# Optimization experiments

Hardware: AMD Instinct MI355X
Metric: run time of the kernel (lower is better)

Reference implementation:

```python
import jax, jax.numpy as jnp
import numpy as np

B, L = 8, 512
D_MODEL, N_HEAD, N_GLOBAL, N_ITER = 64, 8, 64, 4
DAMP_H = 0.0; DAMP_Z = 0.0; STEP_H = 1.0; STEP_Z = 1.0; REG_H = 1.0; REG_Z = 1.0
NEG = -1e9; BIG = 1e9


def sin_pe(length, d):
    # standard additive sinusoidal positional encoding (AddPositionalEncoding)
    pos = np.arange(length, dtype=np.float32)[:, None]
    div = np.exp(np.arange(0, d, 2, dtype=np.float32) * (-np.log(10000.0) / d))
    pe = np.zeros((length, d), dtype=np.float32)
    pe[:, 0::2] = np.sin(pos * div)
    pe[:, 1::2] = np.cos(pos * div)
    return jnp.asarray(pe)


def setup_inputs() -> dict:
    key = jax.random.key(0)
    k1, k2, k3 = jax.random.split(key, 3)
    x = jax.random.normal(k1, (B, L, D_MODEL), jnp.float32)
    mask = jnp.ones((B, L), jnp.int32)
    ternary = jax.random.normal(k2, (D_MODEL, D_MODEL, N_HEAD), jnp.float32)  # std=1 init
    global_w = jax.random.normal(k3, (N_GLOBAL, D_MODEL, 1), jnp.float32) / np.sqrt(D_MODEL)
    return {"x": x, "mask": mask, "ternary": ternary, "global_w": global_w}


def _forward(x, mask, ternary, global_w):
    Bq, Lq, d = x.shape
    norm = lambda a: jax.nn.softmax(a, axis=-1)
    valid = (mask != 0)
    m1 = valid[:, :, None].astype(x.dtype)                      # (B,L,1) keep-mask
    pair = valid[:, None, :, None] & valid[:, None, None, :]    # (B,1,L,L)
    eye_big = BIG * jnp.eye(Lq, dtype=x.dtype)[None, None]      # kill self-edges

    x = x + sin_pe(Lq, d)[None]
    unary = x * m1
    q_z = unary
    q_h1 = jnp.where(pair, 1.0 - eye_big, NEG)                  # (B,H,L,L) via broadcast
    q_h1 = jnp.broadcast_to(q_h1, (Bq, N_HEAD, Lq, Lq))
    q_h2 = jnp.ones((Bq, 1, Lq, N_GLOBAL), x.dtype)             # single-channel: 1 global head

    cache_qh1, cache_qh2 = q_h1, q_h2
    cache_norm_qz = norm(q_z)
    cache_norm_qh1 = norm(q_h1)
    cache_norm_qh2 = norm(q_h2)

    for it in range(N_ITER):
        cache_qz = q_z
        nz = norm(q_z)
        qzn = nz if it == 0 else (1 - STEP_Z) * cache_norm_qz + STEP_Z * nz
        cache_norm_qz = qzn
        qz = qzn * m1
        # F1[z,c,i,j] = sum_{a,b} qz[z,i,a] qz[z,j,b] T[a,b,c]
        t1 = jnp.einsum('zia,abc->zibc', qz, ternary)
        F1 = jnp.einsum('zibc,zjb->zcij', t1, qz)
        F2 = jnp.einsum('zia,jac->zcij', qz, global_w)          # (B,1,L,n_global)
        q_h1 = cache_qh1 * DAMP_H + F1 * (1 - DAMP_H)
        q_h2 = cache_qh2 * DAMP_H + F2 * (1 - DAMP_H)
        cache_qh1, cache_qh2 = q_h1, q_h2
        q_h1m = jnp.where(pair, q_h1 - eye_big, NEG)
        nh1 = norm(q_h1m / REG_H)
        nh2 = norm(q_h2 / REG_H)
        qh1n = nh1 if it == 0 else (1 - STEP_H) * cache_norm_qh1 + STEP_H * nh1
        qh2n = nh2 if it == 0 else (1 - STEP_H) * cache_norm_qh2 + STEP_H * nh2
        cache_norm_qh1, cache_norm_qh2 = qh1n, qh2n
        # messages back to Z: factor (H_i=c, Z_i=a, Z_j=b)
        mi = jnp.einsum('zcij,zjb->zicb', qh1n, qz)
        Mi = jnp.einsum('zicb,abc->zia', mi, ternary)           # to Z_i
        mj = jnp.einsum('zcij,zia->zjca', qh1n, qz)
        Mj = jnp.einsum('zjca,abc->zjb', mj, ternary)           # to Z_j (block_msg=False)
        Mg = jnp.einsum('zcij,jac->zia', qh2n, global_w)        # global-node message
        new_qz = (unary + (Mi + Mj + Mg) / REG_Z) * m1
        q_z = cache_qz * DAMP_Z + new_qz * (1 - DAMP_Z)
    return q_z  # output_prob=False -> unnormalized scores (B,L,d_model)


def reference(x, mask, ternary, global_w):
    return _forward(x, mask, ternary, global_w)
```

## Files before the change

### kernel.cpp

```cpp
#include <hip/hip_runtime.h>

#define BB 8
#define LL 512
#define HH 8
#define BIGV (1e9f)

typedef unsigned short u16;
typedef __attribute__((ext_vector_type(8))) short bf16x8;
typedef __attribute__((ext_vector_type(4))) short s16x4;
typedef __attribute__((ext_vector_type(4))) float f32x4;

#define MFMA(a,b,c) __builtin_amdgcn_mfma_f32_16x16x32_bf16(a,b,c,0,0,0)

__device__ __forceinline__ u16 f2b(float f){
  unsigned u = __float_as_uint(f);
  u = (u + 0x7fffu + ((u>>16)&1u)) >> 16;
  return (u16)u;
}
__device__ __forceinline__ float b2f(u16 s){ return __uint_as_float(((unsigned)s)<<16); }
__device__ __forceinline__ bf16x8 ldb8(const u16* p){ return *(const bf16x8*)p; }
__device__ __forceinline__ s16x4 ld4nt(const u16* p){ return __builtin_nontemporal_load((const s16x4*)p); }

__device__ __forceinline__ float g16_sum(float v){
  v += __shfl_xor(v,1,64); v += __shfl_xor(v,2,64);
  v += __shfl_xor(v,4,64); v += __shfl_xor(v,8,64);
  return v;
}

__global__ void kp_prep(const float* __restrict__ T, const float* __restrict__ gw,
                        u16* __restrict__ T4t, u16* __restrict__ Tt2,
                        u16* __restrict__ Gt, u16* __restrict__ Gt2){
  int idx = blockIdx.x*256 + threadIdx.x;
  { int c=idx>>12, b=(idx>>6)&63, a=idx&63; T4t[idx] = f2b(T[(a*64+b)*8+c]); }
  { int c=idx>>12, a=(idx>>6)&63, b=idx&63; Tt2[idx] = f2b(T[(a*64+b)*8+c]); }
  if(idx < 4096){
    int a=idx>>6, j=idx&63;
    Gt[idx]  = f2b(gw[j*64+a]);
    Gt2[idx] = f2b(gw[idx]);
  }
}

__global__ __launch_bounds__(256) void kCA(const float* __restrict__ x, const int* __restrict__ mask,
      const u16* __restrict__ miP, const u16* __restrict__ mjP, const float* __restrict__ MgF_in,
      float* __restrict__ unary, float* __restrict__ mf,
      const u16* __restrict__ Gt2, const u16* __restrict__ Gt,
      u16* __restrict__ qzb, float* __restrict__ MgF_out, float* __restrict__ out, int mode){
  __shared__ u16 qlds[16*72];
  __shared__ u16 P2s[16*72];
  __shared__ float red2[16*4];
  int bid = blockIdx.x; int z = bid & 7, itile = bid >> 3;
  int t = threadIdx.x, lane = t&63, w = t>>6, l15 = lane&15, lhi = lane>>4;
  int rbase = z*LL + itile*16;
  {
    int row16 = t>>4, c4 = t&15;
    int rg = rbase + row16;
    float v[4]; float mk;
    if(mode == 0){
      mk = (mask[rg] != 0) ? 1.f : 0.f;
      if(c4 == 0) mf[rg] = mk;
      int pos = rg & (LL-1);
      #pragma unroll
      for(int k=0;k<4;k++){
        int d = c4*4 + k;
        float div = __expf(-(float)(d & ~1) * 0.14391156962f);
        float arg = (float)pos * div;
        float pe = (d & 1) ? cosf(arg) : sinf(arg);
        v[k] = (x[(size_t)rg*64 + d] + pe) * mk;
      }
      *(f32x4*)&unary[(size_t)rg*64 + c4*4] = (f32x4){v[0],v[1],v[2],v[3]};
    } else {
      mk = mf[rg];
      f32x4 acc = *(const f32x4*)&MgF_in[(size_t)rg*64 + c4*4];
      #pragma unroll
      for(int c=0;c<8;c++){
        s16x4 vv = ld4nt(&miP[(size_t)rg*512 + c*64 + c4*4]);
        acc[0]+=b2f((u16)vv[0]); acc[1]+=b2f((u16)vv[1]);
        acc[2]+=b2f((u16)vv[2]); acc[3]+=b2f((u16)vv[3]);
      }
      #pragma unroll
      for(int s=0;s<4;s++)
        #pragma unroll
        for(int c=0;c<8;c++){
          s16x4 vv = ld4nt(&mjP[(((size_t)(s*8+z))*LL + itile*16 + row16)*512 + c*64 + c4*4]);
          acc[0]+=b2f((u16)vv[0]); acc[1]+=b2f((u16)vv[1]);
          acc[2]+=b2f((u16)vv[2]); acc[3]+=b2f((u16)vv[3]);
        }
      f32x4 u0 = *(const f32x4*)&unary[(size_t)rg*64 + c4*4];
      #pragma unroll
      for(int k=0;k<4;k++) v[k] = (u0[k] + acc[k]) * mk;
    }
    if(mode == 2){
      *(f32x4*)&out[(size_t)rg*64 + c4*4] = (f32x4){v[0],v[1],v[2],v[3]};
      return;
    }
    float mx = fmaxf(fmaxf(v[0],v[1]), fmaxf(v[2],v[3]));
    mx = fmaxf(mx, __shfl_xor(mx,1,64));
    mx = fmaxf(mx, __shfl_xor(mx,2,64));
    mx = fmaxf(mx, __shfl_xor(mx,4,64));
    mx = fmaxf(mx, __shfl_xor(mx,8,64));
    float s = 0.f;
    #pragma unroll
    for(int k=0;k<4;k++){ v[k] = __expf(v[k]-mx); s += v[k]; }
    s += __shfl_xor(s,1,64); s += __shfl_xor(s,2,64);
    s += __shfl_xor(s,4,64); s += __shfl_xor(s,8,64);
    float iv = mk / s;
    s16x4 q4 = { (short)f2b(v[0]*iv), (short)f2b(v[1]*iv),
                 (short)f2b(v[2]*iv), (short)f2b(v[3]*iv) };
    *(s16x4*)&qzb[(size_t)rg*64 + c4*4] = q4;
    *(s16x4*)&qlds[row16*72 + c4*4] = q4;
  }
  __syncthreads();
  float fv[4];
  {
    bf16x8 a0 = ldb8(&qlds[l15*72 + lhi*8]);
    bf16x8 a1 = ldb8(&qlds[l15*72 + lhi*8 + 32]);
    const u16* Br = Gt2 + (size_t)(w*16 + l15)*64 + lhi*8;
    f32x4 acc = {0.f,0.f,0.f,0.f};
    acc = MFMA(a0, ldb8(Br), acc);
    acc = MFMA(a1, ldb8(Br+32), acc);
    #pragma unroll
    for(int jj=0;jj<4;jj++){
      float e = __expf(acc[jj]);
      fv[jj] = e;
      float p = g16_sum(e);
      if(l15==0) red2[(lhi*4+jj)*4 + w] = p;
    }
  }
  __syncthreads();
  #pragma unroll
  for(int jj=0;jj<4;jj++){
    int r = lhi*4+jj;
    float s = red2[r*4+0]+red2[r*4+1]+red2[r*4+2]+red2[r*4+3];
    float iv = 1.f/s;
    P2s[r*72 + w*16 + l15] = f2b(fv[jj]*iv);
  }
  __syncthreads();
  {
    bf16x8 a0 = ldb8(&P2s[l15*72 + lhi*8]);
    bf16x8 a1 = ldb8(&P2s[l15*72 + lhi*8 + 32]);
    const u16* Br = Gt + (size_t)(w*16 + l15)*64 + lhi*8;
    f32x4 acc = {0.f,0.f,0.f,0.f};
    acc = MFMA(a0, ldb8(Br), acc);
    acc = MFMA(a1, ldb8(Br+32), acc);
    #pragma unroll
    for(int jj=0;jj<4;jj++)
      MgF_out[((size_t)rbase + lhi*4 + jj)*64 + w*16 + l15] = acc[jj];
  }
}

__global__ __launch_bounds__(256) void k2(const u16* __restrict__ qzb,
      const u16* __restrict__ T4t, const u16* __restrict__ Tt2,
      u16* __restrict__ t1b, u16* __restrict__ t1t, u16* __restrict__ t2t){
  __shared__ u16 s1[64*72];
  __shared__ u16 s2[64*72];
  __shared__ u16 s3[64*72];
  int bid = blockIdx.x; int z = bid&7, c = (bid>>3)&7, itile = bid>>6;
  int zc = z*8 + c;
  int t = threadIdx.x, lane = t&63, w = t>>6, l15 = lane&15, lhi = lane>>4;
  int i0 = itile*64;
  const u16* qA = qzb + ((size_t)z*LL + i0 + w*16 + l15)*64 + lhi*8;
  bf16x8 qa0 = ldb8(qA), qa1 = ldb8(qA+32);
  const u16* tA = T4t + c*4096 + (w*16 + l15)*64 + lhi*8;
  bf16x8 ta0 = ldb8(tA), ta1 = ldb8(tA+32);
  const u16* uA = Tt2 + c*4096 + (w*16 + l15)*64 + lhi*8;
  bf16x8 ua0 = ldb8(uA), ua1 = ldb8(uA+32);
  #pragma unroll
  for(int nt=0;nt<4;nt++){
    {
      const u16* Br = T4t + c*4096 + (nt*16 + l15)*64 + lhi*8;
      f32x4 acc = {0.f,0.f,0.f,0.f};
      acc = MFMA(qa0, ldb8(Br), acc);
      acc = MFMA(qa1, ldb8(Br+32), acc);
      #pragma unroll
      for(int jj=0;jj<4;jj++)
        s1[(w*16 + lhi*4 + jj)*72 + nt*16 + l15] = f2b(acc[jj]);
    }
    const u16* Br = qzb + ((size_t)z*LL + i0 + nt*16 + l15)*64 + lhi*8;
    bf16x8 qb0 = ldb8(Br), qb1 = ldb8(Br+32);
    {
      f32x4 acc = {0.f,0.f,0.f,0.f};
      acc = MFMA(ta0, qb0, acc);
      acc = MFMA(ta1, qb1, acc);
      #pragma unroll
      for(int jj=0;jj<4;jj++)
        s2[(w*16 + lhi*4 + jj)*72 + nt*16 + l15] = f2b(acc[jj]);
    }
    {
      f32x4 acc = {0.f,0.f,0.f,0.f};
      acc = MFMA(ua0, qb0, acc);
      acc = MFMA(ua1, qb1, acc);
      #pragma unroll
      for(int jj=0;jj<4;jj++)
        s3[(w*16 + lhi*4 + jj)*72 + nt*16 + l15] = f2b(acc[jj]);
    }
  }
  __syncthreads();
  #pragma unroll
  for(int p=0;p<2;p++){
    int r = p*32 + (t>>3), ch = t&7;
    *(bf16x8*)&t1b[((size_t)zc*LL + i0 + r)*64 + ch*8]   = *(const bf16x8*)&s1[r*72 + ch*8];
    *(bf16x8*)&t1t[((size_t)zc*64 + r)*LL + i0 + ch*8]   = *(const bf16x8*)&s2[r*72 + ch*8];
    *(bf16x8*)&t2t[((size_t)zc*64 + r)*LL + i0 + ch*8]   = *(const bf16x8*)&s3[r*72 + ch*8];
  }
}

__global__ __launch_bounds__(1024) void kF(const u16* __restrict__ t1b, const u16* __restrict__ qzb,
        const u16* __restrict__ t1t, const u16* __restrict__ t2t, const float* __restrict__ mf,
        u16* __restrict__ miP, u16* __restrict__ mjP){
  extern __shared__ char smem[];
  u16*   t2s  = (u16*)smem;
  u16*   Pp   = (u16*)(smem + 66560);
  u16*   PpT  = (u16*)(smem + 99840);
  float* redS2= (float*)(smem + 140800);
  float* stgf = (float*)(smem + 141056);
  u16*   stg  = (u16*)smem;
  int bid = blockIdx.x;
  int z = bid&7, c = (bid>>3)&7, it = bid>>6;
  int zc = z*8 + c;
  int t = threadIdx.x, lane = t&63, w = t>>6, l15 = lane&15, lhi = lane>>4;
  int jc0 = w*32;
  int h = w>>3, wr = (w>>2)&1, wc = w&3;
  if(t < 64) redS2[t] = 0.f;
  __syncthreads();
  #pragma unroll
  for(int m=0;m<4;m++){
    int e = (m*1024 + t)*8;
    int a = e >> 9, j = e & 511;
    *(bf16x8*)&t2s[a*520 + j] = ldb8(t2t + ((size_t)zc*64 + a)*LL + j);
  }
  float mfj[2];
  mfj[0] = mf[z*LL + jc0 + l15];
  mfj[1] = mf[z*LL + jc0 + 16 + l15];
  f32x4 mj[2][4];
  #pragma unroll
  for(int jt=0;jt<2;jt++)
    #pragma unroll
    for(int bt=0;bt<4;bt++) mj[jt][bt] = (f32x4){0.f,0.f,0.f,0.f};
  u16* PpTw = PpT + w*32*40;

  for(int ip=0; ip<4; ++ip){
    int i0g = it*128 + ip*32;
    int par = ip & 1;
    f32x4 S[2][2];
    #pragma unroll
    for(int rt=0;rt<2;rt++){ S[rt][0] = (f32x4){0,0,0,0}; S[rt][1] = (f32x4){0,0,0,0}; }
    #pragma unroll
    for(int rt=0;rt<2;rt++){
      const u16* Ar = t1b + ((size_t)zc*LL + i0g + rt*16 + l15)*64 + lhi*8;
      bf16x8 a0 = ldb8(Ar), a1 = ldb8(Ar+32);
      #pragma unroll
      for(int ct=0;ct<2;ct++){
        const u16* Br = qzb + ((size_t)z*LL + jc0 + ct*16 + l15)*64 + lhi*8;
        S[rt][ct] = MFMA(a0, ldb8(Br), S[rt][ct]);
        S[rt][ct] = MFMA(a1, ldb8(Br+32), S[rt][ct]);
      }
    }
    #pragma unroll
    for(int rt=0;rt<2;rt++)
      #pragma unroll
      for(int jj=0;jj<4;jj++){
        int rloc = rt*16 + lhi*4 + jj;
        int irow = i0g + rloc;
        float mfi = mf[z*LL + irow];
        float ps = 0.f;
        #pragma unroll
        for(int ct=0;ct<2;ct++){
          int jcol = jc0 + ct*16 + l15;
          float v = S[rt][ct][jj] - ((irow==jcol)?BIGV:0.f);
          float e = mfi * mfj[ct] * __expf(v);
          S[rt][ct][jj] = e; ps += e;
          Pp[rloc*520 + jcol] = f2b(e);
        }
        ps = g16_sum(ps);
        if(l15 == 0) atomicAdd(&redS2[par*32 + rloc], ps);
      }
    __syncthreads();
    if(t < 32) redS2[(par^1)*32 + t] = 0.f;
    float ivv[2][4];
    #pragma unroll
    for(int rt=0;rt<2;rt++)
      #pragma unroll
      for(int jj=0;jj<4;jj++){
        float s = redS2[par*32 + rt*16 + lhi*4 + jj];
        ivv[rt][jj] = s > 0.f ? 1.f/s : 0.f;
      }
    #pragma unroll
    for(int rt=0;rt<2;rt++)
      #pragma unroll
      for(int ct=0;ct<2;ct++){
        s16x4 v4 = { (short)f2b(S[rt][ct][0]*ivv[rt][0]), (short)f2b(S[rt][ct][1]*ivv[rt][1]),
                     (short)f2b(S[rt][ct][2]*ivv[rt][2]), (short)f2b(S[rt][ct][3]*ivv[rt][3]) };
        *(s16x4*)&PpTw[(ct*16 + l15)*40 + rt*16 + lhi*4] = v4;
      }
    {
      f32x4 mia = {0.f,0.f,0.f,0.f};
      const u16* Ab = Pp + (wr*16 + l15)*520 + h*256 + lhi*8;
      const u16* Bb = t2s + (wc*16 + l15)*520 + h*256 + lhi*8;
      #pragma unroll
      for(int ks=0;ks<8;ks++)
        mia = MFMA(ldb8(Ab + ks*32), ldb8(Bb + ks*32), mia);
      #pragma unroll
      for(int jj=0;jj<4;jj++)
        stgf[(h*32 + wr*16 + lhi*4 + jj)*68 + wc*16 + l15] = mia[jj]*ivv[wr][jj];
    }
    {
      bf16x8 av[2];
      #pragma unroll
      for(int jt=0;jt<2;jt++)
        av[jt] = ldb8(PpTw + (jt*16 + l15)*40 + lhi*8);
      #pragma unroll
      for(int bt=0;bt<4;bt++){
        bf16x8 b = ldb8(t1t + ((size_t)zc*64 + bt*16 + l15)*LL + i0g + lhi*8);
        #pragma unroll
        for(int jt=0;jt<2;jt++) mj[jt][bt] = MFMA(av[jt], b, mj[jt][bt]);
      }
    }
    __syncthreads();
    if(t < 512){
      int r = t>>4, cc = t&15;
      f32x4 v0 = *(const f32x4*)&stgf[r*68 + cc*4];
      f32x4 v1 = *(const f32x4*)&stgf[(32+r)*68 + cc*4];
      s16x4 o = { (short)f2b(v0[0]+v1[0]), (short)f2b(v0[1]+v1[1]),
                  (short)f2b(v0[2]+v1[2]), (short)f2b(v0[3]+v1[3]) };
      *(s16x4*)&miP[((size_t)z*LL + i0g + r)*512 + c*64 + cc*4] = o;
    }
  }
  #pragma unroll
  for(int jt=0;jt<2;jt++)
    #pragma unroll
    for(int bt=0;bt<4;bt++)
      #pragma unroll
      for(int jj=0;jj<4;jj++)
        stg[(jc0 + jt*16 + lhi*4 + jj)*72 + bt*16 + l15] = f2b(mj[jt][bt][jj]);
  __syncthreads();
  #pragma unroll
  for(int q=0;q<4;q++){
    int e = q*1024 + t;
    int j = e >> 3, ch = e & 7;
    *(bf16x8*)&mjP[(((size_t)(it*8 + z))*LL + j)*512 + c*64 + ch*8]
      = *(const bf16x8*)&stg[j*72 + ch*8];
  }
}

extern "C" void kernel_launch(void* const* d_in, const int* in_sizes, int n_in,
                              void* d_out, int out_size, void* d_ws, size_t ws_size,
                              hipStream_t stream) {
  const float* x       = (const float*)d_in[0];
  const int*   mask    = (const int*)d_in[1];
  const float* ternary = (const float*)d_in[2];
  const float* gw      = (const float*)d_in[3];
  float* out = (float*)d_out;

  const size_t NE = (size_t)BB*LL*64;
  char* p = (char*)d_ws;
  auto alloc = [&](size_t bytes)->void*{
    void* r = (void*)p; p += (bytes + 255) & ~(size_t)255; return r;
  };
  float* unary   = (float*)alloc(NE*4);
  float* mf      = (float*)alloc((size_t)BB*LL*4);
  u16*   qzb     = (u16*)alloc(NE*2);
  u16*   t1b     = (u16*)alloc((size_t)BB*HH*LL*64*2);
  u16*   t1t     = (u16*)alloc((size_t)BB*HH*LL*64*2);
  u16*   t2t     = (u16*)alloc((size_t)BB*HH*LL*64*2);
  float* MgF     = (float*)alloc(NE*4);
  u16*   miP     = (u16*)alloc((size_t)BB*LL*512*2);
  u16*   mjP     = (u16*)alloc((size_t)32*LL*512*2);
  u16*   T4t     = (u16*)alloc(32768*2);
  u16*   Tt2     = (u16*)alloc(32768*2);
  u16*   Gt      = (u16*)alloc(4096*2);
  u16*   Gt2     = (u16*)alloc(4096*2);

  const int KF_LDS = 158464;
  hipFuncSetAttribute(reinterpret_cast<const void*>(kF),
                      hipFuncAttributeMaxDynamicSharedMemorySize, KF_LDS);

  kp_prep<<<128, 256, 0, stream>>>(ternary, gw, T4t, Tt2, Gt, Gt2);
  kCA<<<256, 256, 0, stream>>>(x, mask, miP, mjP, MgF, unary, mf, Gt2, Gt,
                               qzb, MgF, out, 0);
  for(int it=0; it<4; ++it){
    k2<<<512, 256, 0, stream>>>(qzb, T4t, Tt2, t1b, t1t, t2t);
    kF<<<256, 1024, KF_LDS, stream>>>(t1b, qzb, t1t, t2t, mf, miP, mjP);
    kCA<<<256, 256, 0, stream>>>(x, mask, miP, mjP, MgF, unary, mf, Gt2, Gt,
                                 qzb, MgF, out, (it==3) ? 2 : 1);
  }
}
```

Baseline: 218.8 us.

## Fuse t1/t2 projection kernel into softmax kernel kCA using 512 threads

```diff
diff --git a/kernel.cpp b/kernel.cpp
--- a/kernel.cpp
+++ b/kernel.cpp
@@ -40,18 +40,20 @@
   }
 }
 
-__global__ __launch_bounds__(256) void kCA(const float* __restrict__ x, const int* __restrict__ mask,
+__global__ __launch_bounds__(512) void kCA(const float* __restrict__ x, const int* __restrict__ mask,
       const u16* __restrict__ miP, const u16* __restrict__ mjP, const float* __restrict__ MgF_in,
       float* __restrict__ unary, float* __restrict__ mf,
       const u16* __restrict__ Gt2, const u16* __restrict__ Gt,
-      u16* __restrict__ qzb, float* __restrict__ MgF_out, float* __restrict__ out, int mode){
+      const u16* __restrict__ T4t, const u16* __restrict__ Tt2,
+      u16* __restrict__ qzb, float* __restrict__ MgF_out, float* __restrict__ out,
+      u16* __restrict__ t1b, u16* __restrict__ t1t, u16* __restrict__ t2t, int mode){
   __shared__ u16 qlds[16*72];
   __shared__ u16 P2s[16*72];
   __shared__ float red2[16*4];
   int bid = blockIdx.x; int z = bid & 7, itile = bid >> 3;
   int t = threadIdx.x, lane = t&63, w = t>>6, l15 = lane&15, lhi = lane>>4;
   int rbase = z*LL + itile*16;
-  {
+  if(t < 256){
     int row16 = t>>4, c4 = t&15;
     int rg = rbase + row16;
     float v[4]; float mk;
@@ -91,27 +93,28 @@
     }
     if(mode == 2){
       *(f32x4*)&out[(size_t)rg*64 + c4*4] = (f32x4){v[0],v[1],v[2],v[3]};
-      return;
-    }
-    float mx = fmaxf(fmaxf(v[0],v[1]), fmaxf(v[2],v[3]));
-    mx = fmaxf(mx, __shfl_xor(mx,1,64));
-    mx = fmaxf(mx, __shfl_xor(mx,2,64));
-    mx = fmaxf(mx, __shfl_xor(mx,4,64));
-    mx = fmaxf(mx, __shfl_xor(mx,8,64));
-    float s = 0.f;
-    #pragma unroll
-    for(int k=0;k<4;k++){ v[k] = __expf(v[k]-mx); s += v[k]; }
-    s += __shfl_xor(s,1,64); s += __shfl_xor(s,2,64);
-    s += __shfl_xor(s,4,64); s += __shfl_xor(s,8,64);
-    float iv = mk / s;
-    s16x4 q4 = { (short)f2b(v[0]*iv), (short)f2b(v[1]*iv),
-                 (short)f2b(v[2]*iv), (short)f2b(v[3]*iv) };
-    *(s16x4*)&qzb[(size_t)rg*64 + c4*4] = q4;
-    *(s16x4*)&qlds[row16*72 + c4*4] = q4;
-  }
+    } else {
+      float mx = fmaxf(fmaxf(v[0],v[1]), fmaxf(v[2],v[3]));
+      mx = fmaxf(mx, __shfl_xor(mx,1,64));
+      mx = fmaxf(mx, __shfl_xor(mx,2,64));
+      mx = fmaxf(mx, __shfl_xor(mx,4,64));
+      mx = fmaxf(mx, __shfl_xor(mx,8,64));
+      float s = 0.f;
+      #pragma unroll
+      for(int k=0;k<4;k++){ v[k] = __expf(v[k]-mx); s += v[k]; }
+      s += __shfl_xor(s,1,64); s += __shfl_xor(s,2,64);
+      s += __shfl_xor(s,4,64); s += __shfl_xor(s,8,64);
+      float iv = mk / s;
+      s16x4 q4 = { (short)f2b(v[0]*iv), (short)f2b(v[1]*iv),
+                   (short)f2b(v[2]*iv), (short)f2b(v[3]*iv) };
+      *(s16x4*)&qzb[(size_t)rg*64 + c4*4] = q4;
+      *(s16x4*)&qlds[row16*72 + c4*4] = q4;
+    }
+  }
+  if(mode == 2) return;
   __syncthreads();
   float fv[4];
-  {
+  if(t < 256){
     bf16x8 a0 = ldb8(&qlds[l15*72 + lhi*8]);
     bf16x8 a1 = ldb8(&qlds[l15*72 + lhi*8 + 32]);
     const u16* Br = Gt2 + (size_t)(w*16 + l15)*64 + lhi*8;
@@ -127,15 +130,17 @@
     }
   }
   __syncthreads();
-  #pragma unroll
-  for(int jj=0;jj<4;jj++){
-    int r = lhi*4+jj;
-    float s = red2[r*4+0]+red2[r*4+1]+red2[r*4+2]+red2[r*4+3];
-    float iv = 1.f/s;
-    P2s[r*72 + w*16 + l15] = f2b(fv[jj]*iv);
-  }
-  __syncthreads();
-  {
+  if(t < 256){
+    #pragma unroll
+    for(int jj=0;jj<4;jj++){
+      int r = lhi*4+jj;
+      float s = red2[r*4+0]+red2[r*4+1]+red2[r*4+2]+red2[r*4+3];
+      float iv = 1.f/s;
+      P2s[r*72 + w*16 + l15] = f2b(fv[jj]*iv);
+    }
+  }
+  __syncthreads();
+  if(t < 256){
     bf16x8 a0 = ldb8(&P2s[l15*72 + lhi*8]);
     bf16x8 a1 = ldb8(&P2s[l15*72 + lhi*8 + 32]);
     const u16* Br = Gt + (size_t)(w*16 + l15)*64 + lhi*8;
@@ -146,61 +151,36 @@
     for(int jj=0;jj<4;jj++)
       MgF_out[((size_t)rbase + lhi*4 + jj)*64 + w*16 + l15] = acc[jj];
   }
-}
-
-__global__ __launch_bounds__(256) void k2(const u16* __restrict__ qzb,
-      const u16* __restrict__ T4t, const u16* __restrict__ Tt2,
-      u16* __restrict__ t1b, u16* __restrict__ t1t, u16* __restrict__ t2t){
-  __shared__ u16 s1[64*72];
-  __shared__ u16 s2[64*72];
-  __shared__ u16 s3[64*72];
-  int bid = blockIdx.x; int z = bid&7, c = (bid>>3)&7, itile = bid>>6;
-  int zc = z*8 + c;
-  int t = threadIdx.x, lane = t&63, w = t>>6, l15 = lane&15, lhi = lane>>4;
-  int i0 = itile*64;
-  const u16* qA = qzb + ((size_t)z*LL + i0 + w*16 + l15)*64 + lhi*8;
-  bf16x8 qa0 = ldb8(qA), qa1 = ldb8(qA+32);
-  const u16* tA = T4t + c*4096 + (w*16 + l15)*64 + lhi*8;
-  bf16x8 ta0 = ldb8(tA), ta1 = ldb8(tA+32);
-  const u16* uA = Tt2 + c*4096 + (w*16 + l15)*64 + lhi*8;
-  bf16x8 ua0 = ldb8(uA), ua1 = ldb8(uA+32);
-  #pragma unroll
-  for(int nt=0;nt<4;nt++){
-    {
-      const u16* Br = T4t + c*4096 + (nt*16 + l15)*64 + lhi*8;
-      f32x4 acc = {0.f,0.f,0.f,0.f};
-      acc = MFMA(qa0, ldb8(Br), acc);
-      acc = MFMA(qa1, ldb8(Br+32), acc);
-      #pragma unroll
-      for(int jj=0;jj<4;jj++)
-        s1[(w*16 + lhi*4 + jj)*72 + nt*16 + l15] = f2b(acc[jj]);
-    }
-    const u16* Br = qzb + ((size_t)z*LL + i0 + nt*16 + l15)*64 + lhi*8;
-    bf16x8 qb0 = ldb8(Br), qb1 = ldb8(Br+32);
-    {
-      f32x4 acc = {0.f,0.f,0.f,0.f};
-      acc = MFMA(ta0, qb0, acc);
-      acc = MFMA(ta1, qb1, acc);
-      #pragma unroll
-      for(int jj=0;jj<4;jj++)
-        s2[(w*16 + lhi*4 + jj)*72 + nt*16 + l15] = f2b(acc[jj]);
-    }
-    {
-      f32x4 acc = {0.f,0.f,0.f,0.f};
-      acc = MFMA(ua0, qb0, acc);
-      acc = MFMA(ua1, qb1, acc);
-      #pragma unroll
-      for(int jj=0;jj<4;jj++)
-        s3[(w*16 + lhi*4 + jj)*72 + nt*16 + l15] = f2b(acc[jj]);
-    }
-  }
-  __syncthreads();
-  #pragma unroll
-  for(int p=0;p<2;p++){
-    int r = p*32 + (t>>3), ch = t&7;
-    *(bf16x8*)&t1b[((size_t)zc*LL + i0 + r)*64 + ch*8]   = *(const bf16x8*)&s1[r*72 + ch*8];
-    *(bf16x8*)&t1t[((size_t)zc*64 + r)*LL + i0 + ch*8]   = *(const bf16x8*)&s2[r*72 + ch*8];
-    *(bf16x8*)&t2t[((size_t)zc*64 + r)*LL + i0 + ch*8]   = *(const bf16x8*)&s3[r*72 + ch*8];
+  {
+    int c = w;
+    size_t zc = (size_t)z*8 + c;
+    bf16x8 aq0 = ldb8(&qlds[l15*72 + lhi*8]);
+    bf16x8 aq1 = ldb8(&qlds[l15*72 + lhi*8 + 32]);
+    const u16* T4c = T4t + c*4096;
+    const u16* Ttc = Tt2 + c*4096;
+    #pragma unroll
+    for(int s=0;s<4;s++){
+      const u16* Bq = T4c + (s*16 + l15)*64 + lhi*8;
+      bf16x8 tb0 = ldb8(Bq), tb1 = ldb8(Bq+32);
+      const u16* Uq = Ttc + (s*16 + l15)*64 + lhi*8;
+      bf16x8 ub0 = ldb8(Uq), ub1 = ldb8(Uq+32);
+      f32x4 d1 = {0.f,0.f,0.f,0.f};
+      d1 = MFMA(aq0, tb0, d1);
+      d1 = MFMA(aq1, tb1, d1);
+      f32x4 d2 = {0.f,0.f,0.f,0.f};
+      d2 = MFMA(tb0, aq0, d2);
+      d2 = MFMA(tb1, aq1, d2);
+      f32x4 d3 = {0.f,0.f,0.f,0.f};
+      d3 = MFMA(ub0, aq0, d3);
+      d3 = MFMA(ub1, aq1, d3);
+      #pragma unroll
+      for(int jj=0;jj<4;jj++){
+        int r4 = lhi*4 + jj;
+        t1b[(zc*LL + itile*16 + r4)*64 + s*16 + l15]  = f2b(d1[jj]);
+        t1t[(zc*64 + s*16 + r4)*LL + itile*16 + l15]  = f2b(d2[jj]);
+        t2t[(zc*64 + s*16 + r4)*LL + itile*16 + l15]  = f2b(d3[jj]);
+      }
+    }
   }
 }
 
@@ -375,12 +355,11 @@
                       hipFuncAttributeMaxDynamicSharedMemorySize, KF_LDS);
 
   kp_prep<<<128, 256, 0, stream>>>(ternary, gw, T4t, Tt2, Gt, Gt2);
-  kCA<<<256, 256, 0, stream>>>(x, mask, miP, mjP, MgF, unary, mf, Gt2, Gt,
-                               qzb, MgF, out, 0);
+  kCA<<<256, 512, 0, stream>>>(x, mask, miP, mjP, MgF, unary, mf, Gt2, Gt,
+                               T4t, Tt2, qzb, MgF, out, t1b, t1t, t2t, 0);
   for(int it=0; it<4; ++it){
-    k2<<<512, 256, 0, stream>>>(qzb, T4t, Tt2, t1b, t1t, t2t);
     kF<<<256, 1024, KF_LDS, stream>>>(t1b, qzb, t1t, t2t, mf, miP, mjP);
-    kCA<<<256, 256, 0, stream>>>(x, mask, miP, mjP, MgF, unary, mf, Gt2, Gt,
-                                 qzb, MgF, out, (it==3) ? 2 : 1);
-  }
-}
+    kCA<<<256, 512, 0, stream>>>(x, mask, miP, mjP, MgF, unary, mf, Gt2, Gt,
+                                 T4t, Tt2, qzb, MgF, out, t1b, t1t, t2t, (it==3) ? 2 : 1);
+  }
+}
```

New measurement: 208.4 us (median of 2 runs). -4.8%, faster.
